# Optimization experiments

Measured on AMD Instinct MI355X. Metric: run time of the kernel, lower is better.

## Reference

```python
import jax, jax.numpy as jnp
import numpy as np

B, IN_DIM, MEM = 8192, 4096, 256
MIN_TS, MAX_TS, EPS = 0.1, 10.0, 1e-6
LN_EPS = 1e-5


def setup_inputs() -> dict:
    key = jax.random.key(0)
    ks = jax.random.split(key, 10)
    std = 0.02
    d_in = MEM + IN_DIM  # 4352
    return {
        "x": jax.random.normal(ks[0], (B, IN_DIM), jnp.float32),
        "h": jax.random.normal(ks[1], (B, MEM), jnp.float32),
        # memory_target: Linear(d_in, 2*MEM) -> LN -> GELU -> Linear(2*MEM, MEM)
        "W1": std * jax.random.normal(ks[2], (d_in, 2 * MEM), jnp.float32),
        "b1": jnp.zeros((2 * MEM,), jnp.float32),
        "g1": jnp.ones((2 * MEM,), jnp.float32),
        "be1": jnp.zeros((2 * MEM,), jnp.float32),
        "W2": std * jax.random.normal(ks[3], (2 * MEM, MEM), jnp.float32),
        "b2": jnp.zeros((MEM,), jnp.float32),
        # decay_gate: Linear(d_in, MEM) -> sigmoid
        "Wd": std * jax.random.normal(ks[4], (d_in, MEM), jnp.float32),
        "bd": jnp.zeros((MEM,), jnp.float32),
        # input_gate: Linear(d_in, MEM) -> sigmoid
        "Wu": std * jax.random.normal(ks[5], (d_in, MEM), jnp.float32),
        "bu": jnp.zeros((MEM,), jnp.float32),
    }


def _layernorm(t, g, b):
    mu = jnp.mean(t, axis=-1, keepdims=True)
    var = jnp.mean(jnp.square(t - mu), axis=-1, keepdims=True)
    return (t - mu) * jax.lax.rsqrt(var + LN_EPS) * g + b


def reference(x, h, W1, b1, g1, be1, W2, b2, Wd, bd, Wu, bu):
    combined = jnp.concatenate([h, x], axis=-1)  # [B, MEM+IN_DIM]
    # memory_target branch: Linear -> LayerNorm -> GELU (exact) -> Linear -> tanh
    t = _layernorm(combined @ W1 + b1, g1, be1)
    t = jax.nn.gelu(t, approximate=False)
    h_candidate = jnp.tanh(t @ W2 + b2)  # [B, MEM]
    # gates
    decay = jax.nn.sigmoid(combined @ Wd + bd)
    update = jax.nn.sigmoid(combined @ Wu + bu)
    decay = MIN_TS + (MAX_TS - MIN_TS) * decay + EPS
    new_h = (1.0 - update) * (h / decay) + update * h_candidate
    # normalize_memory: rescale new_h to old h's L2 norm
    h_norm = jnp.maximum(jnp.linalg.norm(h, axis=-1, keepdims=True), EPS)
    nh_norm = jnp.maximum(jnp.linalg.norm(new_h, axis=-1, keepdims=True), 1e-12)
    new_h = new_h / nh_norm * h_norm
    return new_h
```

## Files before the change

### kernel.cpp

```cpp
#include <hip/hip_runtime.h>
#include <stdint.h>

typedef unsigned short u16;

#define B_ROWS 8192
#define IN_DIM 4096
#define MEM 256
#define D_IN 4352
#define N1 1024
#define K2 512
#define LN_EPS 1e-5f

typedef __attribute__((ext_vector_type(4))) float f32x4;
typedef __attribute__((ext_vector_type(4))) uint32_t u32x4;
typedef __attribute__((ext_vector_type(4))) unsigned short u16x4;
typedef __attribute__((ext_vector_type(8))) short bf16x8;

#define AS1(p) ((__attribute__((address_space(1))) void*)(p))
#define AS3(p) ((__attribute__((address_space(3))) void*)(p))

__device__ __forceinline__ float bf2f(u16 u) {
  union { uint32_t u; float f; } c; c.u = ((uint32_t)u) << 16; return c.f;
}
__device__ __forceinline__ u16 f2bf(float f) {
  union { float f; uint32_t u; } c; c.f = f;
  uint32_t r = (c.u + 0x7fffu + ((c.u >> 16) & 1u)) >> 16;
  return (u16)r;
}
__device__ __forceinline__ uint32_t fbits(float f) {
  union { float f; uint32_t u; } c; c.f = f; return c.u;
}
__device__ __forceinline__ uint32_t pack_rne(float a, float b) {
  return ((uint32_t)f2bf(b) << 16) | f2bf(a);
}
__device__ __forceinline__ uint32_t pack_trunc(float a, float b) {
  return (fbits(b) & 0xFFFF0000u) | (fbits(a) >> 16);
}

__global__ __launch_bounds__(256)
void cast_A_kernel(const float* __restrict__ h, const float* __restrict__ x,
                   u16* __restrict__ Abf) {
  int b = blockIdx.x, t = threadIdx.x;
  const float* src; int r, c, dcol;
  if (b < 1024) {
    int g = (b * 256 + t) * 8;
    src = h + g; r = g >> 8; c = g & 255; dcol = c;
  } else {
    int g = ((b - 1024) * 256 + t) * 8;
    src = x + g; r = g >> 12; c = g & 4095; dcol = MEM + c;
  }
  f32x4 v0 = *(const f32x4*)src;
  f32x4 v1 = *(const f32x4*)(src + 4);
  u32x4 w;
  w.x = pack_rne(v0[0], v0[1]);
  w.y = pack_rne(v0[2], v0[3]);
  w.z = pack_rne(v1[0], v1[1]);
  w.w = pack_rne(v1[2], v1[3]);
  *(u32x4*)&Abf[(size_t)r * D_IN + dcol] = w;
}

__global__ __launch_bounds__(256)
void transpose_cast_fused(const float* __restrict__ W1, const float* __restrict__ Wd,
                          const float* __restrict__ Wu, u16* __restrict__ WT) {
  __shared__ u16 tile[64][68];
  int n0 = blockIdx.x * 64, k0 = blockIdx.y * 64;
  const float* src; int srcN, ns0;
  if (n0 < 512)      { src = W1; srcN = 512; ns0 = n0; }
  else if (n0 < 768) { src = Wd; srcN = 256; ns0 = n0 - 512; }
  else               { src = Wu; srcN = 256; ns0 = n0 - 768; }
  int t = threadIdx.x;
  int rr = t >> 4;
  int c4 = (t & 15) * 4;
#pragma unroll
  for (int i = 0; i < 4; i++) {
    int k = i * 16 + rr;
    f32x4 v = *(const f32x4*)&src[(size_t)(k0 + k) * srcN + ns0 + c4];
    tile[c4 + 0][k] = f2bf(v[0]);
    tile[c4 + 1][k] = f2bf(v[1]);
    tile[c4 + 2][k] = f2bf(v[2]);
    tile[c4 + 3][k] = f2bf(v[3]);
  }
  __syncthreads();
#pragma unroll
  for (int i = 0; i < 4; i++) {
    int n = i * 16 + rr;
    u16x4 w;
    w.x = tile[n][c4 + 0];
    w.y = tile[n][c4 + 1];
    w.z = tile[n][c4 + 2];
    w.w = tile[n][c4 + 3];
    *(u16x4*)&WT[(size_t)(n0 + n) * D_IN + k0 + c4] = w;
  }
}

__global__ void transpose_cast(const float* __restrict__ src, u16* __restrict__ dst,
                               int K, int N) {
  __shared__ u16 tile[32][34];
  int n0 = blockIdx.x * 32, k0 = blockIdx.y * 32;
  int tx = threadIdx.x, ty = threadIdx.y;
#pragma unroll
  for (int i = 0; i < 4; i++)
    tile[ty + i * 8][tx] = f2bf(src[(size_t)(k0 + ty + i * 8) * N + n0 + tx]);
  __syncthreads();
#pragma unroll
  for (int i = 0; i < 4; i++)
    dst[(size_t)(n0 + ty + i * 8) * K + k0 + tx] = tile[tx][ty + i * 8];
}

__global__ __launch_bounds__(256, 4)
void gemm1_pre_kernel(const u16* __restrict__ Abf, const u16* __restrict__ WT,
                      u16* __restrict__ G0, u16* __restrict__ G1, int klen) {
  __shared__ __attribute__((aligned(16))) u16 As[128 * 64];
  __shared__ __attribute__((aligned(16))) u16 Bs[128 * 64];
  const int t = threadIdx.x;
  const int lane = t & 63, wave = t >> 6;
  const int by = blockIdx.x & 63;
  const int bx = (blockIdx.x >> 6) & 7;
  const int part = blockIdx.x >> 9;
  const int kbase = part * klen;
  u16* __restrict__ Gout = part ? G1 : G0;
  const int row0 = by * 128, col0 = bx * 128;
  const int q = lane >> 4, mrow = lane & 15;
  const int wm = wave >> 1, wn = wave & 1;

  int ar[4], ac[4];
#pragma unroll
  for (int j = 0; j < 4; j++) {
    int idx = j * 256 + t;
    int r = idx >> 3;
    ar[j] = r;
    ac[j] = (idx & 7) ^ (r & 7);
  }

  f32x4 acc[4][4] = {};

  for (int k0 = kbase; k0 < kbase + klen; k0 += 64) {
#pragma unroll
    for (int j = 0; j < 4; j++) {
      const u16* gp = WT + (size_t)(col0 + ar[j]) * D_IN + k0 + ac[j] * 8;
      __builtin_amdgcn_global_load_lds(AS1(gp), AS3(&Bs[(j * 256 + t) * 8]), 16, 0, 0);
    }
#pragma unroll
    for (int j = 0; j < 4; j++) {
      const u16* gp = Abf + (size_t)(row0 + ar[j]) * D_IN + k0 + ac[j] * 8;
      __builtin_amdgcn_global_load_lds(AS1(gp), AS3(&As[(j * 256 + t) * 8]), 16, 0, 0);
    }
    __syncthreads();
#pragma unroll
    for (int kk = 0; kk < 2; kk++) {
      bf16x8 a[4], b[4];
#pragma unroll
      for (int mt = 0; mt < 4; mt++) {
        int row = wm * 64 + mt * 16 + mrow;
        int p = (kk * 4 + q) ^ (mrow & 7);
        a[mt] = *(const bf16x8*)&As[row * 64 + p * 8];
      }
#pragma unroll
      for (int nt = 0; nt < 4; nt++) {
        int row = wn * 64 + nt * 16 + mrow;
        int p = (kk * 4 + q) ^ (mrow & 7);
        b[nt] = *(const bf16x8*)&Bs[row * 64 + p * 8];
      }
#pragma unroll
      for (int mt = 0; mt < 4; mt++) {
#pragma unroll
        for (int nt = 0; nt < 4; nt++) {
          acc[mt][nt] = __builtin_amdgcn_mfma_f32_16x16x32_bf16(a[mt], b[nt], acc[mt][nt], 0, 0, 0);
        }
      }
    }
    __syncthreads();
  }
#pragma unroll
  for (int mt = 0; mt < 4; mt++) {
#pragma unroll
    for (int nt = 0; nt < 4; nt++) {
#pragma unroll
      for (int i = 0; i < 4; i++) {
        int row = row0 + wm * 64 + mt * 16 + q * 4 + i;
        int col = col0 + wn * 64 + nt * 16 + mrow;
        Gout[(size_t)row * N1 + col] = f2bf(acc[mt][nt][i]);
      }
    }
  }
}

__global__ __launch_bounds__(256, 4)
void gemm1_inline_kernel(const float* __restrict__ x, const float* __restrict__ h,
                         const u16* __restrict__ WT, u16* __restrict__ G0,
                         u16* __restrict__ G1, int klen) {
  __shared__ __attribute__((aligned(16))) u16 As[128 * 64];
  __shared__ __attribute__((aligned(16))) u16 Bs[128 * 64];
  const int t = threadIdx.x;
  const int lane = t & 63, wave = t >> 6;
  const int by = blockIdx.x & 63;
  const int bx = (blockIdx.x >> 6) & 7;
  const int part = blockIdx.x >> 9;
  const int kbase = part * klen;
  u16* __restrict__ Gout = part ? G1 : G0;
  const int row0 = by * 128, col0 = bx * 128;
  const int q = lane >> 4, mrow = lane & 15;
  const int wm = wave >> 1, wn = wave & 1;

  int ar[4], ac[4];
#pragma unroll
  for (int j = 0; j < 4; j++) {
    int idx = j * 256 + t;
    int r = idx >> 3;
    ar[j] = r;
    ac[j] = (idx & 7) ^ (r & 7);
  }
  f32x4 acc[4][4] = {};
  for (int k0 = kbase; k0 < kbase + klen; k0 += 64) {
#pragma unroll
    for (int j = 0; j < 4; j++) {
      const u16* gp = WT + (size_t)(col0 + ar[j]) * D_IN + k0 + ac[j] * 8;
      __builtin_amdgcn_global_load_lds(AS1(gp), AS3(&Bs[(j * 256 + t) * 8]), 16, 0, 0);
    }
#pragma unroll
    for (int j = 0; j < 4; j++) {
      int k = k0 + ac[j] * 8;
      const float* gp = (k < MEM) ? (h + (size_t)(row0 + ar[j]) * MEM + k)
                                  : (x + (size_t)(row0 + ar[j]) * IN_DIM + (k - MEM));
      f32x4 v0 = *(const f32x4*)gp;
      f32x4 v1 = *(const f32x4*)(gp + 4);
      u32x4 w;
      w.x = pack_trunc(v0[0], v0[1]);
      w.y = pack_trunc(v0[2], v0[3]);
      w.z = pack_trunc(v1[0], v1[1]);
      w.w = pack_trunc(v1[2], v1[3]);
      *(u32x4*)&As[(j * 256 + t) * 8] = w;
    }
    __syncthreads();
#pragma unroll
    for (int kk = 0; kk < 2; kk++) {
      bf16x8 a[4], b[4];
#pragma unroll
      for (int mt = 0; mt < 4; mt++) {
        int row = wm * 64 + mt * 16 + mrow;
        int p = (kk * 4 + q) ^ (mrow & 7);
        a[mt] = *(const bf16x8*)&As[row * 64 + p * 8];
      }
#pragma unroll
      for (int nt = 0; nt < 4; nt++) {
        int row = wn * 64 + nt * 16 + mrow;
        int p = (kk * 4 + q) ^ (mrow & 7);
        b[nt] = *(const bf16x8*)&Bs[row * 64 + p * 8];
      }
#pragma unroll
      for (int mt = 0; mt < 4; mt++) {
#pragma unroll
        for (int nt = 0; nt < 4; nt++) {
          acc[mt][nt] = __builtin_amdgcn_mfma_f32_16x16x32_bf16(a[mt], b[nt], acc[mt][nt], 0, 0, 0);
        }
      }
    }
    __syncthreads();
  }
#pragma unroll
  for (int mt = 0; mt < 4; mt++) {
#pragma unroll
    for (int nt = 0; nt < 4; nt++) {
#pragma unroll
      for (int i = 0; i < 4; i++) {
        int row = row0 + wm * 64 + mt * 16 + q * 4 + i;
        int col = col0 + wn * 64 + nt * 16 + mrow;
        Gout[(size_t)row * N1 + col] = f2bf(acc[mt][nt][i]);
      }
    }
  }
}

__global__ __launch_bounds__(256, 2)
void fused_ln_gemm2_kernel(const u16* __restrict__ G0, const u16* __restrict__ G1,
                           const u16* __restrict__ W2T, const float* __restrict__ h,
                           const float* __restrict__ b1v, const float* __restrict__ g1v,
                           const float* __restrict__ be1v, const float* __restrict__ b2,
                           const float* __restrict__ bd, const float* __restrict__ bu,
                           float* __restrict__ out, int nparts) {
  __shared__ __attribute__((aligned(16))) u16 As[16 * 512];
  __shared__ __attribute__((aligned(16))) u16 Bs[256 * 64];
  __shared__ float redA[16][4], redB[16][4], scl[16];
  const int t = threadIdx.x, lane = t & 63, wave = t >> 6;
  const int q = lane >> 4, mrow = lane & 15;
  const int r0 = blockIdx.x * 16;

  {
    const int lr = t & 15;
    const int lc = t >> 4;
    float z[32];
    const u16* g0p = G0 + (size_t)(r0 + lr) * N1 + lc * 32;
    const u16* g1p = G1 + (size_t)(r0 + lr) * N1 + lc * 32;
    float s = 0.f, ss = 0.f;
#pragma unroll
    for (int j = 0; j < 4; j++) {
      u32x4 w0 = *(const u32x4*)(g0p + j * 8);
      u32x4 w1;
      if (nparts == 2) w1 = *(const u32x4*)(g1p + j * 8);
#pragma unroll
      for (int e = 0; e < 4; e++) {
        float lo = bf2f((u16)(w0[e] & 0xffff));
        float hi = bf2f((u16)(w0[e] >> 16));
        if (nparts == 2) {
          lo += bf2f((u16)(w1[e] & 0xffff));
          hi += bf2f((u16)(w1[e] >> 16));
        }
        int cb = lc * 32 + j * 8 + e * 2;
        lo += b1v[cb];
        hi += b1v[cb + 1];
        z[j * 8 + e * 2] = lo;
        z[j * 8 + e * 2 + 1] = hi;
        s += lo + hi;
        ss += lo * lo + hi * hi;
      }
    }
    s += __shfl_xor(s, 16, 64);  s += __shfl_xor(s, 32, 64);
    ss += __shfl_xor(ss, 16, 64); ss += __shfl_xor(ss, 32, 64);
    if (lane < 16) { redA[lr][wave] = s; redB[lr][wave] = ss; }
    __syncthreads();
    float S  = redA[lr][0] + redA[lr][1] + redA[lr][2] + redA[lr][3];
    float SS = redB[lr][0] + redB[lr][1] + redB[lr][2] + redB[lr][3];
    float mu = S * (1.0f / 512.0f);
    float var = SS * (1.0f / 512.0f) - mu * mu;
    float rstd = rsqrtf(var + LN_EPS);
#pragma unroll
    for (int j = 0; j < 4; j++) {
      u32x4 wpk;
#pragma unroll
      for (int e = 0; e < 4; e++) {
        int cb = lc * 32 + j * 8 + e * 2;
        float y0 = (z[j * 8 + e * 2] - mu) * rstd * g1v[cb] + be1v[cb];
        float y1 = (z[j * 8 + e * 2 + 1] - mu) * rstd * g1v[cb + 1] + be1v[cb + 1];
        float o0 = 0.5f * y0 * (1.0f + erff(y0 * 0.7071067811865475f));
        float o1 = 0.5f * y1 * (1.0f + erff(y1 * 0.7071067811865475f));
        wpk[e] = pack_rne(o0, o1);
      }
      int p = lc * 4 + j;
      int ps = p ^ (lr & 7);
      *(u32x4*)&As[lr * 512 + ps * 8] = wpk;
    }
  }

  int brB[8], bcB[8];
#pragma unroll
  for (int j = 0; j < 8; j++) {
    int idx = j * 256 + t;
    brB[j] = idx >> 3;
    bcB[j] = (idx & 7) ^ (brB[j] & 7);
  }
  f32x4 acc[4] = {};
  for (int k0 = 0; k0 < K2; k0 += 64) {
#pragma unroll
    for (int j = 0; j < 8; j++) {
      __builtin_amdgcn_global_load_lds(AS1(W2T + (size_t)brB[j] * K2 + k0 + bcB[j] * 8),
                                       AS3(&Bs[(j * 256 + t) * 8]), 16, 0, 0);
    }
    __syncthreads();
#pragma unroll
    for (int kk = 0; kk < 2; kk++) {
      int kw = (k0 >> 5) + kk;
      int pa = (kw * 4 + q) ^ (mrow & 7);
      bf16x8 a = *(const bf16x8*)&As[mrow * 512 + pa * 8];
      bf16x8 b[4];
#pragma unroll
      for (int nt = 0; nt < 4; nt++) {
        int row = wave * 64 + nt * 16 + mrow;
        int p = (kk * 4 + q) ^ (row & 7);
        b[nt] = *(const bf16x8*)&Bs[row * 64 + p * 8];
      }
#pragma unroll
      for (int nt = 0; nt < 4; nt++) {
        acc[nt] = __builtin_amdgcn_mfma_f32_16x16x32_bf16(a, b[nt], acc[nt], 0, 0, 0);
      }
    }
    __syncthreads();
  }

  float snh[4], shh[4];
#pragma unroll
  for (int i = 0; i < 4; i++) {
    int r = q * 4 + i;
    size_t grow = (size_t)(r0 + r);
    float a_nh = 0.f, a_h = 0.f;
#pragma unroll
    for (int nt = 0; nt < 4; nt++) {
      int c = wave * 64 + nt * 16 + mrow;
      float hc = tanhf(acc[nt][i] + b2[c]);
      float zd = bf2f(G0[grow * N1 + 512 + c]);
      float zu = bf2f(G0[grow * N1 + 768 + c]);
      if (nparts == 2) {
        zd += bf2f(G1[grow * N1 + 512 + c]);
        zu += bf2f(G1[grow * N1 + 768 + c]);
      }
      zd += bd[c];
      zu += bu[c];
      float dec = 0.1f + 9.9f / (1.0f + expf(-zd)) + 1e-6f;
      float u = 1.0f / (1.0f + expf(-zu));
      float hv = h[grow * MEM + c];
      float nh = (1.0f - u) * (hv / dec) + u * hc;
      acc[nt][i] = nh;
      a_nh += nh * nh;
      a_h += hv * hv;
    }
    snh[i] = a_nh;
    shh[i] = a_h;
  }
#pragma unroll
  for (int m = 1; m <= 8; m <<= 1) {
#pragma unroll
    for (int i = 0; i < 4; i++) {
      snh[i] += __shfl_xor(snh[i], m, 64);
      shh[i] += __shfl_xor(shh[i], m, 64);
    }
  }
  if (mrow == 0) {
#pragma unroll
    for (int i = 0; i < 4; i++) {
      int r = q * 4 + i;
      redA[r][wave] = snh[i];
      redB[r][wave] = shh[i];
    }
  }
  __syncthreads();
  if (t < 16) {
    float tn = redA[t][0] + redA[t][1] + redA[t][2] + redA[t][3];
    float th = redB[t][0] + redB[t][1] + redB[t][2] + redB[t][3];
    float hn = fmaxf(sqrtf(th), 1e-6f);
    float nn = fmaxf(sqrtf(tn), 1e-12f);
    scl[t] = hn / nn;
  }
  __syncthreads();
#pragma unroll
  for (int i = 0; i < 4; i++) {
    int r = q * 4 + i;
    size_t grow = (size_t)(r0 + r);
    float sc = scl[r];
#pragma unroll
    for (int nt = 0; nt < 4; nt++) {
      int c = wave * 64 + nt * 16 + mrow;
      out[grow * MEM + c] = acc[nt][i] * sc;
    }
  }
}

extern "C" void kernel_launch(void* const* d_in, const int* in_sizes, int n_in,
                              void* d_out, int out_size, void* d_ws, size_t ws_size,
                              hipStream_t stream) {
  const float* x   = (const float*)d_in[0];
  const float* h   = (const float*)d_in[1];
  const float* W1  = (const float*)d_in[2];
  const float* b1  = (const float*)d_in[3];
  const float* g1  = (const float*)d_in[4];
  const float* be1 = (const float*)d_in[5];
  const float* W2  = (const float*)d_in[6];
  const float* b2  = (const float*)d_in[7];
  const float* Wd  = (const float*)d_in[8];
  const float* bd  = (const float*)d_in[9];
  const float* Wu  = (const float*)d_in[10];
  const float* bu  = (const float*)d_in[11];
  float* out = (float*)d_out;

  char* ws = (char*)d_ws;
  u16* WT  = (u16*)(ws);
  u16* W2T = (u16*)(ws + 8912896);
  u16* G0  = (u16*)(ws + 9175040);
  u16* G1  = (u16*)(ws + 25952256);
  u16* Abf = (u16*)(ws + 42729472);

  const int nparts = (ws_size >= 42729472u) ? 2 : 1;
  const int klen = D_IN / nparts;
  const bool use_pre = (ws_size >= 114032640u);

  transpose_cast_fused<<<dim3(N1 / 64, D_IN / 64), 256, 0, stream>>>(W1, Wd, Wu, WT);
  transpose_cast<<<dim3(256 / 32, 512 / 32), dim3(32, 8), 0, stream>>>(W2, W2T, 512, 256);

  if (use_pre) {
    cast_A_kernel<<<17408, 256, 0, stream>>>(h, x, Abf);
    gemm1_pre_kernel<<<512 * nparts, 256, 0, stream>>>(Abf, WT, G0, G1, klen);
  } else {
    gemm1_inline_kernel<<<512 * nparts, 256, 0, stream>>>(x, h, WT, G0, G1, klen);
  }

  fused_ln_gemm2_kernel<<<B_ROWS / 16, 256, 0, stream>>>(G0, G1, W2T, h, b1, g1, be1,
                                                         b2, bd, bu, out, nparts);
}
```

Measured before the change: 343.2 us.

## Merge prep kernels and read pre-fragmented W2 directly from global in GEMM2

Fuses the W1/Wd/Wu transpose-cast, the W2 cast and the activation cast into one prep kernel, removing two launches. W2 is now stored in an MFMA-fragment-ready layout, so the LN+GEMM2 kernel loads B operands straight from global/L2 with no LDS staging or per-K-step barriers. Dropping the 32KB Bs buffer lets launch bounds rise to 4 blocks per CU. The trade is that every block re-reads W2 from cache rather than sharing it through LDS.

```diff
diff --git a/kernel.cpp b/kernel.cpp
--- a/kernel.cpp
+++ b/kernel.cpp
@@ -38,73 +38,74 @@
 }
 
 __global__ __launch_bounds__(256)
-void cast_A_kernel(const float* __restrict__ h, const float* __restrict__ x,
-                   u16* __restrict__ Abf) {
-  int b = blockIdx.x, t = threadIdx.x;
-  const float* src; int r, c, dcol;
-  if (b < 1024) {
-    int g = (b * 256 + t) * 8;
-    src = h + g; r = g >> 8; c = g & 255; dcol = c;
+void prep_kernel(const float* __restrict__ W1, const float* __restrict__ Wd,
+                 const float* __restrict__ Wu, const float* __restrict__ W2,
+                 const float* __restrict__ h, const float* __restrict__ x,
+                 u16* __restrict__ WT, u16* __restrict__ W2F, u16* __restrict__ Abf) {
+  __shared__ u16 tile[64][68];
+  const int blk = blockIdx.x, t = threadIdx.x;
+  if (blk < 1088) {
+    int n0 = (blk & 15) * 64, k0 = (blk >> 4) * 64;
+    const float* src; int srcN, ns0;
+    if (n0 < 512)      { src = W1; srcN = 512; ns0 = n0; }
+    else if (n0 < 768) { src = Wd; srcN = 256; ns0 = n0 - 512; }
+    else               { src = Wu; srcN = 256; ns0 = n0 - 768; }
+    int rr = t >> 4;
+    int c4 = (t & 15) * 4;
+#pragma unroll
+    for (int i = 0; i < 4; i++) {
+      int k = i * 16 + rr;
+      f32x4 v = *(const f32x4*)&src[(size_t)(k0 + k) * srcN + ns0 + c4];
+      tile[c4 + 0][k] = f2bf(v[0]);
+      tile[c4 + 1][k] = f2bf(v[1]);
+      tile[c4 + 2][k] = f2bf(v[2]);
+      tile[c4 + 3][k] = f2bf(v[3]);
+    }
+    __syncthreads();
+#pragma unroll
+    for (int i = 0; i < 4; i++) {
+      int n = i * 16 + rr;
+      u16x4 w;
+      w.x = tile[n][c4 + 0];
+      w.y = tile[n][c4 + 1];
+      w.z = tile[n][c4 + 2];
+      w.w = tile[n][c4 + 3];
+      *(u16x4*)&WT[(size_t)(n0 + n) * D_IN + k0 + c4] = w;
+    }
+  } else if (blk < 1104) {
+    int kw = blk - 1088;
+#pragma unroll
+    for (int q = 0; q < 4; q++) {
+      float v[8];
+#pragma unroll
+      for (int j = 0; j < 8; j++)
+        v[j] = W2[(size_t)(kw * 32 + q * 8 + j) * 256 + t];
+      u32x4 w;
+      w.x = pack_rne(v[0], v[1]);
+      w.y = pack_rne(v[2], v[3]);
+      w.z = pack_rne(v[4], v[5]);
+      w.w = pack_rne(v[6], v[7]);
+      *(u32x4*)&W2F[(size_t)((kw * 4 + q) * 256 + t) * 8] = w;
+    }
   } else {
-    int g = ((b - 1024) * 256 + t) * 8;
-    src = x + g; r = g >> 12; c = g & 4095; dcol = MEM + c;
-  }
-  f32x4 v0 = *(const f32x4*)src;
-  f32x4 v1 = *(const f32x4*)(src + 4);
-  u32x4 w;
-  w.x = pack_rne(v0[0], v0[1]);
-  w.y = pack_rne(v0[2], v0[3]);
-  w.z = pack_rne(v1[0], v1[1]);
-  w.w = pack_rne(v1[2], v1[3]);
-  *(u32x4*)&Abf[(size_t)r * D_IN + dcol] = w;
-}
-
-__global__ __launch_bounds__(256)
-void transpose_cast_fused(const float* __restrict__ W1, const float* __restrict__ Wd,
-                          const float* __restrict__ Wu, u16* __restrict__ WT) {
-  __shared__ u16 tile[64][68];
-  int n0 = blockIdx.x * 64, k0 = blockIdx.y * 64;
-  const float* src; int srcN, ns0;
-  if (n0 < 512)      { src = W1; srcN = 512; ns0 = n0; }
-  else if (n0 < 768) { src = Wd; srcN = 256; ns0 = n0 - 512; }
-  else               { src = Wu; srcN = 256; ns0 = n0 - 768; }
-  int t = threadIdx.x;
-  int rr = t >> 4;
-  int c4 = (t & 15) * 4;
-#pragma unroll
-  for (int i = 0; i < 4; i++) {
-    int k = i * 16 + rr;
-    f32x4 v = *(const f32x4*)&src[(size_t)(k0 + k) * srcN + ns0 + c4];
-    tile[c4 + 0][k] = f2bf(v[0]);
-    tile[c4 + 1][k] = f2bf(v[1]);
-    tile[c4 + 2][k] = f2bf(v[2]);
-    tile[c4 + 3][k] = f2bf(v[3]);
-  }
-  __syncthreads();
-#pragma unroll
-  for (int i = 0; i < 4; i++) {
-    int n = i * 16 + rr;
-    u16x4 w;
-    w.x = tile[n][c4 + 0];
-    w.y = tile[n][c4 + 1];
-    w.z = tile[n][c4 + 2];
-    w.w = tile[n][c4 + 3];
-    *(u16x4*)&WT[(size_t)(n0 + n) * D_IN + k0 + c4] = w;
-  }
-}
-
-__global__ void transpose_cast(const float* __restrict__ src, u16* __restrict__ dst,
-                               int K, int N) {
-  __shared__ u16 tile[32][34];
-  int n0 = blockIdx.x * 32, k0 = blockIdx.y * 32;
-  int tx = threadIdx.x, ty = threadIdx.y;
-#pragma unroll
-  for (int i = 0; i < 4; i++)
-    tile[ty + i * 8][tx] = f2bf(src[(size_t)(k0 + ty + i * 8) * N + n0 + tx]);
-  __syncthreads();
-#pragma unroll
-  for (int i = 0; i < 4; i++)
-    dst[(size_t)(n0 + ty + i * 8) * K + k0 + tx] = tile[tx][ty + i * 8];
+    int b = blk - 1104;
+    const float* src; int r, dcol;
+    if (b < 1024) {
+      int g = (b * 256 + t) * 8;
+      src = h + g; r = g >> 8; dcol = g & 255;
+    } else {
+      int g = ((b - 1024) * 256 + t) * 8;
+      src = x + g; r = g >> 12; dcol = MEM + (g & 4095);
+    }
+    f32x4 v0 = *(const f32x4*)src;
+    f32x4 v1 = *(const f32x4*)(src + 4);
+    u32x4 w;
+    w.x = pack_rne(v0[0], v0[1]);
+    w.y = pack_rne(v0[2], v0[3]);
+    w.z = pack_rne(v1[0], v1[1]);
+    w.w = pack_rne(v1[2], v1[3]);
+    *(u32x4*)&Abf[(size_t)r * D_IN + dcol] = w;
+  }
 }
 
 __global__ __launch_bounds__(256, 4)
@@ -271,15 +272,14 @@
   }
 }
 
-__global__ __launch_bounds__(256, 2)
+__global__ __launch_bounds__(256, 4)
 void fused_ln_gemm2_kernel(const u16* __restrict__ G0, const u16* __restrict__ G1,
-                           const u16* __restrict__ W2T, const float* __restrict__ h,
+                           const u16* __restrict__ W2F, const float* __restrict__ h,
                            const float* __restrict__ b1v, const float* __restrict__ g1v,
                            const float* __restrict__ be1v, const float* __restrict__ b2,
                            const float* __restrict__ bd, const float* __restrict__ bu,
                            float* __restrict__ out, int nparts) {
   __shared__ __attribute__((aligned(16))) u16 As[16 * 512];
-  __shared__ __attribute__((aligned(16))) u16 Bs[256 * 64];
   __shared__ float redA[16][4], redB[16][4], scl[16];
   const int t = threadIdx.x, lane = t & 63, wave = t >> 6;
   const int q = lane >> 4, mrow = lane & 15;
@@ -340,41 +340,21 @@
       *(u32x4*)&As[lr * 512 + ps * 8] = wpk;
     }
   }
-
-  int brB[8], bcB[8];
-#pragma unroll
-  for (int j = 0; j < 8; j++) {
-    int idx = j * 256 + t;
-    brB[j] = idx >> 3;
-    bcB[j] = (idx & 7) ^ (brB[j] & 7);
-  }
+  __syncthreads();
+
   f32x4 acc[4] = {};
-  for (int k0 = 0; k0 < K2; k0 += 64) {
-#pragma unroll
-    for (int j = 0; j < 8; j++) {
-      __builtin_amdgcn_global_load_lds(AS1(W2T + (size_t)brB[j] * K2 + k0 + bcB[j] * 8),
-                                       AS3(&Bs[(j * 256 + t) * 8]), 16, 0, 0);
-    }
-    __syncthreads();
-#pragma unroll
-    for (int kk = 0; kk < 2; kk++) {
-      int kw = (k0 >> 5) + kk;
-      int pa = (kw * 4 + q) ^ (mrow & 7);
-      bf16x8 a = *(const bf16x8*)&As[mrow * 512 + pa * 8];
-      bf16x8 b[4];
-#pragma unroll
-      for (int nt = 0; nt < 4; nt++) {
-        int row = wave * 64 + nt * 16 + mrow;
-        int p = (kk * 4 + q) ^ (row & 7);
-        b[nt] = *(const bf16x8*)&Bs[row * 64 + p * 8];
-      }
-#pragma unroll
-      for (int nt = 0; nt < 4; nt++) {
-        acc[nt] = __builtin_amdgcn_mfma_f32_16x16x32_bf16(a, b[nt], acc[nt], 0, 0, 0);
-      }
-    }
-    __syncthreads();
-  }
+#pragma unroll
+  for (int kw = 0; kw < 16; kw++) {
+    int pa = (kw * 4 + q) ^ (mrow & 7);
+    bf16x8 a = *(const bf16x8*)&As[mrow * 512 + pa * 8];
+#pragma unroll
+    for (int nt = 0; nt < 4; nt++) {
+      const u16* bp = W2F + (size_t)((kw * 4 + q) * 256 + wave * 64 + nt * 16 + mrow) * 8;
+      bf16x8 b = *(const bf16x8*)bp;
+      acc[nt] = __builtin_amdgcn_mfma_f32_16x16x32_bf16(a, b, acc[nt], 0, 0, 0);
+    }
+  }
+  __syncthreads();
 
   float snh[4], shh[4];
 #pragma unroll
@@ -462,7 +442,7 @@
 
   char* ws = (char*)d_ws;
   u16* WT  = (u16*)(ws);
-  u16* W2T = (u16*)(ws + 8912896);
+  u16* W2F = (u16*)(ws + 8912896);
   u16* G0  = (u16*)(ws + 9175040);
   u16* G1  = (u16*)(ws + 25952256);
   u16* Abf = (u16*)(ws + 42729472);
@@ -471,16 +451,14 @@
   const int klen = D_IN / nparts;
   const bool use_pre = (ws_size >= 114032640u);
 
-  transpose_cast_fused<<<dim3(N1 / 64, D_IN / 64), 256, 0, stream>>>(W1, Wd, Wu, WT);
-  transpose_cast<<<dim3(256 / 32, 512 / 32), dim3(32, 8), 0, stream>>>(W2, W2T, 512, 256);
-
   if (use_pre) {
-    cast_A_kernel<<<17408, 256, 0, stream>>>(h, x, Abf);
+    prep_kernel<<<18512, 256, 0, stream>>>(W1, Wd, Wu, W2, h, x, WT, W2F, Abf);
     gemm1_pre_kernel<<<512 * nparts, 256, 0, stream>>>(Abf, WT, G0, G1, klen);
   } else {
+    prep_kernel<<<1104, 256, 0, stream>>>(W1, Wd, Wu, W2, h, x, WT, W2F, Abf);
     gemm1_inline_kernel<<<512 * nparts, 256, 0, stream>>>(x, h, WT, G0, G1, klen);
   }
 
-  fused_ln_gemm2_kernel<<<B_ROWS / 16, 256, 0, stream>>>(G0, G1, W2T, h, b1, g1, be1,
+  fused_ln_gemm2_kernel<<<B_ROWS / 16, 256, 0, stream>>>(G0, G1, W2F, h, b1, g1, be1,
                                                          b2, bd, bu, out, nparts);
 }
```

After: 337.4 us. Within noise of the previous version (-1.7%).
